# Optimization experiments

Measured on AMD Instinct MI355X. Metric: run time of the kernel, lower is better.

Reference implementation:

```python
import jax, jax.numpy as jnp
import numpy as np

GRID_SIZE = 10
SPLINE_ORDER = 3
GRID_RANGE = (0.0, 1.0)
COUNT_HARMONIC = 8


def make_grid():
    # knot vector: (grid_size + 2*spline_order + 1,) = (17,), same for every input feature
    h = (GRID_RANGE[1] - GRID_RANGE[0]) / GRID_SIZE
    return (jnp.arange(-SPLINE_ORDER, GRID_SIZE + SPLINE_ORDER + 1, dtype=jnp.float32) * h
            + GRID_RANGE[0])


def b_splines(x, grid):
    # x: (B, in) -> bases: (B, in, grid_size + spline_order) via Cox-de Boor recursion
    xg = x[..., None]                                   # (B, in, 1)
    bases = ((xg >= grid[:-1]) & (xg < grid[1:])).astype(x.dtype)  # (B, in, 16)
    for k in range(1, SPLINE_ORDER + 1):
        left = (xg - grid[:-(k + 1)]) / (grid[k:-1] - grid[:-(k + 1)]) * bases[..., :-1]
        right = (grid[k + 1:] - xg) / (grid[k + 1:] - grid[1:-k]) * bases[..., 1:]
        bases = left + right
    return bases                                        # (B, in, 13)


def kan_linear(x, base_w, spline_w, spline_scaler, grid):
    # base path: SiLU(x) @ W_base^T ; spline path: grouped weighted sum of B-spline bases
    base_out = jax.nn.silu(x) @ base_w.T                # (B, out)
    sp = b_splines(x, grid)                             # (B, in, C)
    sw = spline_w * spline_scaler[..., None]            # (out, in, C) standalone scaler
    spline_out = jnp.einsum('bic,oic->bo', sp, sw)
    return base_out + spline_out


def fft_calc(x):
    # x: (B, C, 64); two 32-sample windows, keep first count_harmonic+1 = 9 bins
    prev = jnp.fft.rfft(x[:, :, :32])[:, :, :COUNT_HARMONIC + 1]
    cur = jnp.fft.rfft(x[:, :, 32:])[:, :, :COUNT_HARMONIC + 1]
    # NOTE: original code uses the *current* window's phase twice (faithful to source)
    return jnp.concatenate(
        [jnp.abs(prev), jnp.angle(cur), jnp.abs(cur), jnp.angle(cur)], axis=-1)  # (B, C, 36)


def mlp_head(h, W1, b1, W2, b2, W3, b3):
    y = h @ W1.T + b1
    # nn.LeakyReLU(True) -> negative_slope = 1.0 -> identity (faithful to source)
    y = y @ W2.T + b2
    y = jnp.where(y >= 0, y, 0.05 * y)                  # LeakyReLU(0.05)
    y = y @ W3.T + b3
    return jax.nn.sigmoid(y)                            # (B, 1)


def setup_inputs() -> dict:
    key = jax.random.key(0)
    ks = jax.random.split(key, 20)
    B = 8192
    def n(i, shape):
        return jax.random.normal(ks[i], shape, dtype=jnp.float32)
    return {
        'x': n(0, (B, 64, 14)),
        'k1_base': n(1, (80, 504)), 'k1_spline': n(2, (80, 504, 13)), 'k1_scaler': n(3, (80, 504)),
        'k2_base': n(4, (160, 80)), 'k2_spline': n(5, (160, 80, 13)), 'k2_scaler': n(6, (160, 80)),
        'k3_base': n(7, (80, 160)), 'k3_spline': n(8, (80, 160, 13)), 'k3_scaler': n(9, (80, 160)),
        'k4_base': n(10, (40, 80)), 'k4_spline': n(11, (40, 80, 13)), 'k4_scaler': n(12, (40, 80)),
        'heads_W1': n(13, (3, 40, 40)), 'heads_b1': n(14, (3, 40)),
        'heads_W2': n(15, (3, 20, 40)), 'heads_b2': n(16, (3, 20)),
        'heads_W3': n(17, (3, 1, 20)), 'heads_b3': n(18, (3, 1)),
    }


def reference(x, k1_base, k1_spline, k1_scaler, k2_base, k2_spline, k2_scaler,
              k3_base, k3_spline, k3_scaler, k4_base, k4_spline, k4_scaler,
              heads_W1, heads_b1, heads_W2, heads_b2, heads_W3, heads_b3):
    B = x.shape[0]
    grid = make_grid()
    # original uses reshape (not transpose): (B, 64, 14) -> (B, 14, 64)
    h = x.reshape(B, x.shape[2], x.shape[1])
    h = fft_calc(h).reshape(B, -1)                      # (B, 504)
    h = kan_linear(h, k1_base, k1_spline, k1_scaler, grid)   # (B, 80)
    h = kan_linear(h, k2_base, k2_spline, k2_scaler, grid)   # (B, 160)
    h = kan_linear(h, k3_base, k3_spline, k3_scaler, grid)   # (B, 80)
    h = kan_linear(h, k4_base, k4_spline, k4_scaler, grid)   # (B, 40)
    heads = jax.vmap(lambda W1, b1, W2, b2, W3, b3: mlp_head(h, W1, b1, W2, b2, W3, b3))(
        heads_W1, heads_b1, heads_W2, heads_b2, heads_W3, heads_b3)  # (3, B, 1)
    return jnp.transpose(heads, (1, 0, 2)).reshape(B, 3)
```

## Files before the change

kernel.cpp:

```cpp
#include <hip/hip_runtime.h>
#include <math.h>


__device__ __forceinline__ float silu_f(float x) {
    return x / (1.f + __expf(-x));
}

__global__ __launch_bounds__(128) void fft_kernel(const float* __restrict__ x,
                                                  float* __restrict__ F0, int P) {
    __shared__ float xs[128 * 65];
    __shared__ float twc[288], tws[288];
    int tid = threadIdx.x;
    for (int t = tid; t < 288; t += 128) {
        int k = t >> 5, n = t & 31;
        int m = (k * n) & 31;
        float ang = -0.19634954084936207f * (float)m;
        float s, c;
        sincosf(ang, &s, &c);
        twc[t] = c; tws[t] = s;
    }
    int p0 = blockIdx.x * 128;
    for (int idx = tid; idx < 128 * 64; idx += 128) {
        int g = p0 * 64 + idx;
        float v = (g < P * 64) ? x[g] : 0.f;
        xs[(idx >> 6) * 65 + (idx & 63)] = v;
    }
    __syncthreads();
    int p = p0 + tid;
    if (p >= P) return;
    const float* row = &xs[tid * 65];
    float r[64];
#pragma unroll
    for (int n = 0; n < 64; ++n) r[n] = row[n];
    float outv[27];
#pragma unroll
    for (int k = 0; k < 9; ++k) {
        float rp = 0.f, ip = 0.f, rc = 0.f, ic = 0.f;
#pragma unroll
        for (int n = 0; n < 32; ++n) {
            float c = twc[k * 32 + n], s = tws[k * 32 + n];
            rp = fmaf(r[n], c, rp);
            ip = fmaf(r[n], s, ip);
            rc = fmaf(r[n + 32], c, rc);
            ic = fmaf(r[n + 32], s, ic);
        }
        float ap = sqrtf(fmaf(rp, rp, ip * ip));
        float ac = sqrtf(fmaf(rc, rc, ic * ic));
        float gc = atan2f(ic, rc);
        outv[k] = ap; outv[9 + k] = gc; outv[18 + k] = ac;
    }
    float* dst = &F0[(size_t)p * 27];
#pragma unroll
    for (int q = 0; q < 27; ++q) dst[q] = outv[q];
}

__device__ __forceinline__ float kval(const float* __restrict__ bw,
                                      const float* __restrict__ sw,
                                      const float* __restrict__ sc,
                                      int IN, int o, int s, int c) {
    if (c == 0) return bw[o * IN + s];
    return sw[((size_t)o * IN + s) * 13 + (c - 1)] * sc[o * IN + s];
}

__global__ void prep_all_kernel(float* __restrict__ Wf1, float* __restrict__ Wf2,
                                float* __restrict__ Wf3, float* __restrict__ Wf4,
                                float* __restrict__ W21, float* __restrict__ b21,
                                const float* k1b, const float* k1s, const float* k1c,
                                const float* k2b, const float* k2s, const float* k2c,
                                const float* k3b, const float* k3s, const float* k3c,
                                const float* k4b, const float* k4s, const float* k4c,
                                const float* W1, const float* b1,
                                const float* W2, const float* b2) {
    const int T1 = 378 * 14 * 80, T2 = 80 * 14 * 160, T3 = 160 * 14 * 80, T4 = 80 * 14 * 40;
    int id = blockIdx.x * 256 + threadIdx.x;
    if (id < T1) {
        int o = id % 80, rem = id / 80, c = rem % 14, i = rem / 14;
        int ch = i / 27, q = i % 27;
        int s1 = ch * 36 + q;
        float v = kval(k1b, k1s, k1c, 504, o, s1, c);
        if (q >= 9 && q < 18) v += kval(k1b, k1s, k1c, 504, o, s1 + 18, c);
        Wf1[id] = v;
        return;
    }
    id -= T1;
    if (id < T2) {
        int o = id % 160, rem = id / 160, c = rem % 14, i = rem / 14;
        Wf2[id] = kval(k2b, k2s, k2c, 80, o, i, c);
        return;
    }
    id -= T2;
    if (id < T3) {
        int o = id % 80, rem = id / 80, c = rem % 14, i = rem / 14;
        Wf3[id] = kval(k3b, k3s, k3c, 160, o, i, c);
        return;
    }
    id -= T3;
    if (id < T4) {
        int o = id % 40, rem = id / 40, c = rem % 14, i = rem / 14;
        Wf4[id] = kval(k4b, k4s, k4c, 80, o, i, c);
        return;
    }
    id -= T4;
    if (id < 3 * 20 * 40) {
        int k = id % 40, rem = id / 40, j = rem % 20, h = rem / 20;
        float a = 0.f;
        for (int m = 0; m < 40; ++m)
            a = fmaf(W2[(h * 20 + j) * 40 + m], W1[(h * 40 + m) * 40 + k], a);
        W21[id] = a;
    } else if (id < 3 * 20 * 40 + 60) {
        int t = id - 2400, j = t % 20, h = t / 20;
        float a = b2[h * 20 + j];
        for (int m = 0; m < 40; ++m)
            a = fmaf(W2[(h * 20 + j) * 40 + m], b1[h * 40 + m], a);
        b21[t] = a;
    }
}

template <int OUT_T, int BM, int KC>
__global__ __launch_bounds__(256, 4) void kan4_kernel(const float* __restrict__ X, int IN,
                                                      int OUTF,
                                                      const float* __restrict__ Wf,
                                                      float* __restrict__ Yp, int B) {
    constexpr int NR = 10;
    constexpr int COLS_T = OUT_T / NR;
    constexpr int ROWS_T = 256 / COLS_T;
    constexpr int MR = BM / ROWS_T;
    constexpr int NRP = 12;
    static_assert(COLS_T * NR == OUT_T, "cols");
    static_assert(ROWS_T * MR == BM, "rows");
    static_assert(KC % 2 == 0, "even KC");

    __shared__ float Ws[2 * 14 * COLS_T * NRP];
    __shared__ float Ft[2 * 14 * BM];

    const int tid = threadIdx.x;
    const int ct = tid % COLS_T, rt = tid / COLS_T;
    const int b0 = blockIdx.x * BM;
    const int ibase = blockIdx.y * KC;
    const int co = blockIdx.z * OUT_T;
    const int kk = tid / BM;
    const int rr = tid % BM;
    const bool fact = (kk < 2);

    float acc[MR][NR];
#pragma unroll
    for (int m = 0; m < MR; ++m)
#pragma unroll
        for (int n = 0; n < NR; ++n) acc[m][n] = 0.f;

    float xreg = 0.f;
    if (fact) xreg = X[(size_t)(b0 + rr) * IN + ibase + kk];

    for (int i0 = 0; i0 < KC; i0 += 2) {
        if (fact) {
            float xs = xreg;
            float* dst = &Ft[kk * 14 * BM + rr];
            dst[0] = silu_f(xs);
#pragma unroll
            for (int c = 1; c < 14; ++c) dst[c * BM] = 0.f;
            float t10 = (xs + 0.3f) * 10.f;
            if (t10 >= 0.f && t10 < 16.f) {
                int j = (int)t10;
                float u = t10 - (float)j;
                float u2 = u * u, u3 = u2 * u, v = 1.f - u;
                float B0 = v * v * v * (1.f / 6.f);
                float B1 = (3.f * u3 - 6.f * u2 + 4.f) * (1.f / 6.f);
                float B2 = (-3.f * u3 + 3.f * u2 + 3.f * u + 1.f) * (1.f / 6.f);
                float B3 = u3 * (1.f / 6.f);
                int bs = j - 3;
#pragma unroll
                for (int t = 0; t < 4; ++t) {
                    int rw = bs + t;
                    float bb = (t == 0) ? B0 : (t == 1) ? B1 : (t == 2) ? B2 : B3;
                    if (rw >= 0 && rw <= 12) dst[(1 + rw) * BM] = bb;
                }
            }
        }
        {
            const float* wsrc = Wf + (size_t)(ibase + i0) * 14 * OUTF + co;
            for (int t = tid; t < 2 * 14 * OUT_T; t += 256) {
                int o = t % OUT_T;
                int kc = t / OUT_T;
                Ws[(kc * COLS_T + o / NR) * NRP + (o % NR)] = wsrc[(size_t)kc * OUTF + o];
            }
        }
        float xn = 0.f;
        if (fact && (i0 + 2) < KC)
            xn = X[(size_t)(b0 + rr) * IN + ibase + i0 + 2 + kk];
        __syncthreads();
#pragma unroll
        for (int kc = 0; kc < 28; ++kc) {
            const float* wb = &Ws[(kc * COLS_T + ct) * NRP];
            float4 w0 = *(const float4*)(wb);
            float4 w1 = *(const float4*)(wb + 4);
            float2 w2 = *(const float2*)(wb + 8);
            float wn[NR] = {w0.x, w0.y, w0.z, w0.w, w1.x, w1.y, w1.z, w1.w, w2.x, w2.y};
            const float* fb = &Ft[kc * BM + rt * MR];
            float xm[MR];
            if constexpr (MR == 4) {
                float4 f = *(const float4*)fb;
                xm[0] = f.x; xm[1] = f.y; xm[2] = f.z; xm[3] = f.w;
            } else if constexpr (MR == 2) {
                float2 f = *(const float2*)fb;
                xm[0] = f.x; xm[1] = f.y;
            } else {
                xm[0] = fb[0];
            }
#pragma unroll
            for (int m = 0; m < MR; ++m)
#pragma unroll
                for (int n = 0; n < NR; ++n) acc[m][n] = fmaf(xm[m], wn[n], acc[m][n]);
        }
        __syncthreads();
        xreg = xn;
    }

    float* ydst = Yp + (size_t)blockIdx.y * B * OUTF;
#pragma unroll
    for (int m = 0; m < MR; ++m) {
        float* yr = ydst + (size_t)(b0 + rt * MR + m) * OUTF + co + ct * NR;
#pragma unroll
        for (int nn = 0; nn < NR / 2; ++nn)
            *(float2*)(yr + 2 * nn) = make_float2(acc[m][2 * nn], acc[m][2 * nn + 1]);
    }
}

__global__ void reduce_kernel(float* __restrict__ Y, const float* __restrict__ Yp,
                              int N, int KS) {
    int t = blockIdx.x * 256 + threadIdx.x;
    if (t >= N) return;
    float a = 0.f;
    for (int s = 0; s < KS; ++s) a += Yp[(size_t)s * N + t];
    Y[t] = a;
}

__global__ __launch_bounds__(256) void heads_kernel(const float* __restrict__ h4,
                                                    const float* __restrict__ W21,
                                                    const float* __restrict__ b21,
                                                    const float* __restrict__ W3,
                                                    const float* __restrict__ b3,
                                                    float* __restrict__ out, int B) {
    __shared__ float w21s[2400], b21s[60], w3s[60], b3s[3];
    int tid = threadIdx.x;
    for (int t = tid; t < 2400; t += 256) w21s[t] = W21[t];
    if (tid < 60) { b21s[tid] = b21[tid]; w3s[tid] = W3[tid]; }
    if (tid < 3) b3s[tid] = b3[tid];
    __syncthreads();
    int id = blockIdx.x * 256 + tid;
    if (id >= B * 3) return;
    int b = id / 3, h = id % 3;
    const float* hr = &h4[(size_t)b * 40];
    float hv[40];
#pragma unroll
    for (int m = 0; m < 40; ++m) hv[m] = hr[m];
    float z = b3s[h];
#pragma unroll
    for (int j = 0; j < 20; ++j) {
        float y = b21s[h * 20 + j];
        const float* wr = &w21s[(h * 20 + j) * 40];
#pragma unroll
        for (int m = 0; m < 40; ++m) y = fmaf(wr[m], hv[m], y);
        y = (y >= 0.f) ? y : 0.05f * y;
        z = fmaf(w3s[h * 20 + j], y, z);
    }
    out[id] = 1.f / (1.f + __expf(-z));
}

extern "C" void kernel_launch(void* const* d_in, const int* in_sizes, int n_in,
                              void* d_out, int out_size, void* d_ws, size_t ws_size,
                              hipStream_t stream) {
    const float* x   = (const float*)d_in[0];
    const float* k1b = (const float*)d_in[1];
    const float* k1s = (const float*)d_in[2];
    const float* k1c = (const float*)d_in[3];
    const float* k2b = (const float*)d_in[4];
    const float* k2s = (const float*)d_in[5];
    const float* k2c = (const float*)d_in[6];
    const float* k3b = (const float*)d_in[7];
    const float* k3s = (const float*)d_in[8];
    const float* k3c = (const float*)d_in[9];
    const float* k4b = (const float*)d_in[10];
    const float* k4s = (const float*)d_in[11];
    const float* k4c = (const float*)d_in[12];
    const float* hW1 = (const float*)d_in[13];
    const float* hb1 = (const float*)d_in[14];
    const float* hW2 = (const float*)d_in[15];
    const float* hb2 = (const float*)d_in[16];
    const float* hW3 = (const float*)d_in[17];
    const float* hb3 = (const float*)d_in[18];
    float* out = (float*)d_out;

    int B = in_sizes[0] / (64 * 14);
    int P = B * 14;

    float* ws = (float*)d_ws;
    size_t off = 0;
    float* Wf1 = ws + off; off += 378 * 14 * 80;
    float* Wf2 = ws + off; off += 80 * 14 * 160;
    float* Wf3 = ws + off; off += 160 * 14 * 80;
    float* Wf4 = ws + off; off += 80 * 14 * 40;
    float* W21 = ws + off; off += 2400;
    float* b21 = ws + off; off += 60;
    float* F0  = ws + off; off += (size_t)B * 378;
    float* h1  = ws + off; off += (size_t)B * 80;
    float* h2  = ws + off; off += (size_t)B * 160;
    float* h3  = ws + off; off += (size_t)B * 80;
    float* h4  = ws + off; off += (size_t)B * 40;
    float* Yp  = ws + off;
    size_t cap = (ws_size / 4 > off) ? (ws_size / 4 - off) : 0;

    int S1 = (cap >= (size_t)21 * B * 80)  ? 21 : 9;
    int S2 = (cap >= (size_t)8  * B * 160) ? 8  : 4;
    int S3 = (cap >= (size_t)16 * B * 80)  ? 16 : 8;
    const int S4 = 8;

    {
        int total = 378 * 14 * 80 + 80 * 14 * 160 + 160 * 14 * 80 + 80 * 14 * 40 + 2460;
        prep_all_kernel<<<(total + 255) / 256, 256, 0, stream>>>(
            Wf1, Wf2, Wf3, Wf4, W21, b21,
            k1b, k1s, k1c, k2b, k2s, k2c, k3b, k3s, k3c, k4b, k4s, k4c,
            hW1, hb1, hW2, hb2);
    }

    fft_kernel<<<(P + 127) / 128, 128, 0, stream>>>(x, F0, P);

    if (S1 == 21) kan4_kernel<80, 128, 18><<<dim3(B / 128, 21, 1), 256, 0, stream>>>(F0, 378, 80, Wf1, Yp, B);
    else          kan4_kernel<80, 128, 42><<<dim3(B / 128, 9, 1), 256, 0, stream>>>(F0, 378, 80, Wf1, Yp, B);
    reduce_kernel<<<((B * 80) + 255) / 256, 256, 0, stream>>>(h1, Yp, B * 80, S1);

    if (S2 == 8) kan4_kernel<80, 128, 10><<<dim3(B / 128, 8, 2), 256, 0, stream>>>(h1, 80, 160, Wf2, Yp, B);
    else         kan4_kernel<80, 128, 20><<<dim3(B / 128, 4, 2), 256, 0, stream>>>(h1, 80, 160, Wf2, Yp, B);
    reduce_kernel<<<((B * 160) + 255) / 256, 256, 0, stream>>>(h2, Yp, B * 160, S2);

    if (S3 == 16) kan4_kernel<80, 128, 10><<<dim3(B / 128, 16, 1), 256, 0, stream>>>(h2, 160, 80, Wf3, Yp, B);
    else          kan4_kernel<80, 128, 20><<<dim3(B / 128, 8, 1), 256, 0, stream>>>(h2, 160, 80, Wf3, Yp, B);
    reduce_kernel<<<((B * 80) + 255) / 256, 256, 0, stream>>>(h3, Yp, B * 80, S3);

    kan4_kernel<40, 64, 10><<<dim3(B / 64, S4, 1), 256, 0, stream>>>(h3, 80, 40, Wf4, Yp, B);
    reduce_kernel<<<((B * 40) + 255) / 256, 256, 0, stream>>>(h4, Yp, B * 40, S4);

    heads_kernel<<<(B * 3 + 255) / 256, 256, 0, stream>>>(h4, W21, b21, hW3, hb3, out, B);

    (void)n_in; (void)out_size;
}
```

Measured before the change: 420.7 us.

## Switch KAN layers to feature-major activations with pre-packed, register-prefetched weights

Activations are now stored feature-major (transposed), with a new transpose kernel after the FFT. The KAN kernel reads inputs coalesced along the batch and writes partial outputs transposed with vector stores. Weights are pre-packed in prep into the exact padded shared-memory tile layout, so each chunk is a straight contiguous copy that is prefetched into registers one chunk ahead. The goal is to remove strided activation loads and the index-heavy weight scatter, at the cost of an extra transpose pass, more register pressure, a dropped occupancy hint and changed split counts.

Result: faster. 389.2 us (-7.5%).

```diff
diff --git a/kernel.cpp b/kernel.cpp
--- a/kernel.cpp
+++ b/kernel.cpp
@@ -54,6 +54,20 @@
     for (int q = 0; q < 27; ++q) dst[q] = outv[q];
 }
 
+__global__ __launch_bounds__(256) void transpose_f0_kernel(const float* __restrict__ F0,
+                                                           float* __restrict__ F0T, int B) {
+    __shared__ float t[448 * 27];
+    int b0 = blockIdx.x * 32;
+    const float* src = F0 + (size_t)b0 * 14 * 27;
+    for (int idx = threadIdx.x; idx < 448 * 27; idx += 256) t[idx] = src[idx];
+    __syncthreads();
+    for (int idx = threadIdx.x; idx < 378 * 32; idx += 256) {
+        int i = idx >> 5, bb = idx & 31;
+        int ch = i / 27, q = i - ch * 27;
+        F0T[(size_t)i * B + b0 + bb] = t[(bb * 14 + ch) * 27 + q];
+    }
+}
+
 __device__ __forceinline__ float kval(const float* __restrict__ bw,
                                       const float* __restrict__ sw,
                                       const float* __restrict__ sc,
@@ -62,8 +76,8 @@
     return sw[((size_t)o * IN + s) * 13 + (c - 1)] * sc[o * IN + s];
 }
 
-__global__ void prep_all_kernel(float* __restrict__ Wf1, float* __restrict__ Wf2,
-                                float* __restrict__ Wf3, float* __restrict__ Wf4,
+__global__ void prep_all_kernel(float* __restrict__ Wfp1, float* __restrict__ Wfp2,
+                                float* __restrict__ Wfp3, float* __restrict__ Wfp4,
                                 float* __restrict__ W21, float* __restrict__ b21,
                                 const float* k1b, const float* k1s, const float* k1c,
                                 const float* k2b, const float* k2s, const float* k2c,
@@ -71,34 +85,40 @@
                                 const float* k4b, const float* k4s, const float* k4c,
                                 const float* W1, const float* b1,
                                 const float* W2, const float* b2) {
-    const int T1 = 378 * 14 * 80, T2 = 80 * 14 * 160, T3 = 160 * 14 * 80, T4 = 80 * 14 * 40;
+    const int T1 = 189 * 2688, T2 = 40 * 2 * 2688, T3 = 80 * 2688, T4 = 40 * 1344;
     int id = blockIdx.x * 256 + threadIdx.x;
     if (id < T1) {
-        int o = id % 80, rem = id / 80, c = rem % 14, i = rem / 14;
-        int ch = i / 27, q = i % 27;
-        int s1 = ch * 36 + q;
-        float v = kval(k1b, k1s, k1c, 504, o, s1, c);
-        if (q >= 9 && q < 18) v += kval(k1b, k1s, k1c, 504, o, s1 + 18, c);
-        Wf1[id] = v;
-        return;
+        int jg = id / 2688, t = id % 2688;
+        int kc = t / 96, t2 = t % 96, ct = t2 / 12, r = t2 % 12;
+        int i = 2 * jg + kc / 14, c = kc % 14, o = ct * 10 + r;
+        float v = 0.f;
+        if (r < 10) {
+            int ch = i / 27, q = i - ch * 27, s1 = ch * 36 + q;
+            v = kval(k1b, k1s, k1c, 504, o, s1, c);
+            if (q >= 9 && q < 18) v += kval(k1b, k1s, k1c, 504, o, s1 + 18, c);
+        }
+        Wfp1[id] = v; return;
     }
     id -= T1;
     if (id < T2) {
-        int o = id % 160, rem = id / 160, c = rem % 14, i = rem / 14;
-        Wf2[id] = kval(k2b, k2s, k2c, 80, o, i, c);
-        return;
+        int jg = id / (2 * 2688), rem = id % (2 * 2688), half = rem / 2688, t = rem % 2688;
+        int kc = t / 96, t2 = t % 96, ct = t2 / 12, r = t2 % 12;
+        int i = 2 * jg + kc / 14, c = kc % 14, o = half * 80 + ct * 10 + r;
+        Wfp2[id] = (r < 10) ? kval(k2b, k2s, k2c, 80, o, i, c) : 0.f; return;
     }
     id -= T2;
     if (id < T3) {
-        int o = id % 80, rem = id / 80, c = rem % 14, i = rem / 14;
-        Wf3[id] = kval(k3b, k3s, k3c, 160, o, i, c);
-        return;
+        int jg = id / 2688, t = id % 2688;
+        int kc = t / 96, t2 = t % 96, ct = t2 / 12, r = t2 % 12;
+        int i = 2 * jg + kc / 14, c = kc % 14, o = ct * 10 + r;
+        Wfp3[id] = (r < 10) ? kval(k3b, k3s, k3c, 160, o, i, c) : 0.f; return;
     }
     id -= T3;
     if (id < T4) {
-        int o = id % 40, rem = id / 40, c = rem % 14, i = rem / 14;
-        Wf4[id] = kval(k4b, k4s, k4c, 80, o, i, c);
-        return;
+        int jg = id / 1344, t = id % 1344;
+        int kc = t / 48, t2 = t % 48, ct = t2 / 12, r = t2 % 12;
+        int i = 2 * jg + kc / 14, c = kc % 14, o = ct * 10 + r;
+        Wfp4[id] = (r < 10) ? kval(k4b, k4s, k4c, 80, o, i, c) : 0.f; return;
     }
     id -= T4;
     if (id < 3 * 20 * 40) {
@@ -116,31 +136,33 @@
     }
 }
 
-template <int OUT_T, int BM, int KC>
-__global__ __launch_bounds__(256, 4) void kan4_kernel(const float* __restrict__ X, int IN,
-                                                      int OUTF,
-                                                      const float* __restrict__ Wf,
-                                                      float* __restrict__ Yp, int B) {
+template <int OUT_T, int KC, int NHALF>
+__global__ __launch_bounds__(256) void kan5_kernel(const float* __restrict__ XT, int B,
+                                                   const float* __restrict__ Wfp,
+                                                   float* __restrict__ YpT, int OUTF) {
+    constexpr int BM = 128;
     constexpr int NR = 10;
     constexpr int COLS_T = OUT_T / NR;
     constexpr int ROWS_T = 256 / COLS_T;
     constexpr int MR = BM / ROWS_T;
-    constexpr int NRP = 12;
+    constexpr int NW = 28 * COLS_T * 12;
+    constexpr int NCH = KC / 2;
+    constexpr int WSTG = (NW + 255) / 256;
     static_assert(COLS_T * NR == OUT_T, "cols");
     static_assert(ROWS_T * MR == BM, "rows");
     static_assert(KC % 2 == 0, "even KC");
 
-    __shared__ float Ws[2 * 14 * COLS_T * NRP];
-    __shared__ float Ft[2 * 14 * BM];
+    __shared__ float Ws[NW];
+    __shared__ float Ft[28 * BM];
 
     const int tid = threadIdx.x;
-    const int ct = tid % COLS_T, rt = tid / COLS_T;
+    const int rt = tid % ROWS_T, ct = tid / ROWS_T;
     const int b0 = blockIdx.x * BM;
-    const int ibase = blockIdx.y * KC;
-    const int co = blockIdx.z * OUT_T;
-    const int kk = tid / BM;
-    const int rr = tid % BM;
-    const bool fact = (kk < 2);
+    const int s = blockIdx.y;
+    const int half = blockIdx.z;
+    const int ibase = s * KC;
+    const int kk = tid >> 7;
+    const int rr = tid & 127;
 
     float acc[MR][NR];
 #pragma unroll
@@ -148,11 +170,23 @@
 #pragma unroll
         for (int n = 0; n < NR; ++n) acc[m][n] = 0.f;
 
-    float xreg = 0.f;
-    if (fact) xreg = X[(size_t)(b0 + rr) * IN + ibase + kk];
-
-    for (int i0 = 0; i0 < KC; i0 += 2) {
-        if (fact) {
+    const size_t wbase0 = ((size_t)(ibase / 2) * NHALF + half) * NW;
+    float wreg[WSTG];
+#pragma unroll
+    for (int u = 0; u < WSTG; ++u) {
+        int t = tid + u * 256;
+        wreg[u] = (t < NW) ? Wfp[wbase0 + t] : 0.f;
+    }
+    float xreg = XT[(size_t)(ibase + kk) * B + b0 + rr];
+
+    for (int j = 0; j < NCH; ++j) {
+        __syncthreads();
+#pragma unroll
+        for (int u = 0; u < WSTG; ++u) {
+            int t = tid + u * 256;
+            if (t < NW) Ws[t] = wreg[u];
+        }
+        {
             float xs = xreg;
             float* dst = &Ft[kk * 14 * BM + rr];
             dst[0] = silu_f(xs);
@@ -160,14 +194,14 @@
             for (int c = 1; c < 14; ++c) dst[c * BM] = 0.f;
             float t10 = (xs + 0.3f) * 10.f;
             if (t10 >= 0.f && t10 < 16.f) {
-                int j = (int)t10;
-                float u = t10 - (float)j;
+                int jj = (int)t10;
+                float u = t10 - (float)jj;
                 float u2 = u * u, u3 = u2 * u, v = 1.f - u;
                 float B0 = v * v * v * (1.f / 6.f);
                 float B1 = (3.f * u3 - 6.f * u2 + 4.f) * (1.f / 6.f);
                 float B2 = (-3.f * u3 + 3.f * u2 + 3.f * u + 1.f) * (1.f / 6.f);
                 float B3 = u3 * (1.f / 6.f);
-                int bs = j - 3;
+                int bs = jj - 3;
 #pragma unroll
                 for (int t = 0; t < 4; ++t) {
                     int rw = bs + t;
@@ -176,21 +210,19 @@
                 }
             }
         }
-        {
-            const float* wsrc = Wf + (size_t)(ibase + i0) * 14 * OUTF + co;
-            for (int t = tid; t < 2 * 14 * OUT_T; t += 256) {
-                int o = t % OUT_T;
-                int kc = t / OUT_T;
-                Ws[(kc * COLS_T + o / NR) * NRP + (o % NR)] = wsrc[(size_t)kc * OUTF + o];
+        if (j + 1 < NCH) {
+            const size_t wb = wbase0 + (size_t)(j + 1) * NHALF * NW;
+#pragma unroll
+            for (int u = 0; u < WSTG; ++u) {
+                int t = tid + u * 256;
+                if (t < NW) wreg[u] = Wfp[wb + t];
             }
-        }
-        float xn = 0.f;
-        if (fact && (i0 + 2) < KC)
-            xn = X[(size_t)(b0 + rr) * IN + ibase + i0 + 2 + kk];
+            xreg = XT[(size_t)(ibase + 2 * (j + 1) + kk) * B + b0 + rr];
+        }
         __syncthreads();
 #pragma unroll
         for (int kc = 0; kc < 28; ++kc) {
-            const float* wb = &Ws[(kc * COLS_T + ct) * NRP];
+            const float* wb = &Ws[(kc * COLS_T + ct) * 12];
             float4 w0 = *(const float4*)(wb);
             float4 w1 = *(const float4*)(wb + 4);
             float2 w2 = *(const float2*)(wb + 8);
@@ -200,28 +232,25 @@
             if constexpr (MR == 4) {
                 float4 f = *(const float4*)fb;
                 xm[0] = f.x; xm[1] = f.y; xm[2] = f.z; xm[3] = f.w;
-            } else if constexpr (MR == 2) {
+            } else {
                 float2 f = *(const float2*)fb;
                 xm[0] = f.x; xm[1] = f.y;
-            } else {
-                xm[0] = fb[0];
             }
 #pragma unroll
             for (int m = 0; m < MR; ++m)
 #pragma unroll
                 for (int n = 0; n < NR; ++n) acc[m][n] = fmaf(xm[m], wn[n], acc[m][n]);
         }
-        __syncthreads();
-        xreg = xn;
-    }
-
-    float* ydst = Yp + (size_t)blockIdx.y * B * OUTF;
-#pragma unroll
-    for (int m = 0; m < MR; ++m) {
-        float* yr = ydst + (size_t)(b0 + rt * MR + m) * OUTF + co + ct * NR;
-#pragma unroll
-        for (int nn = 0; nn < NR / 2; ++nn)
-            *(float2*)(yr + 2 * nn) = make_float2(acc[m][2 * nn], acc[m][2 * nn + 1]);
+    }
+
+    float* yd = YpT + (size_t)s * OUTF * B + (size_t)(half * OUT_T) * B;
+#pragma unroll
+    for (int n = 0; n < NR; ++n) {
+        float* p = yd + (size_t)(ct * NR + n) * B + b0 + rt * MR;
+        if constexpr (MR == 4)
+            *(float4*)p = make_float4(acc[0][n], acc[1][n], acc[2][n], acc[3][n]);
+        else
+            *(float2*)p = make_float2(acc[0][n], acc[1][n]);
     }
 }
 
@@ -234,7 +263,7 @@
     Y[t] = a;
 }
 
-__global__ __launch_bounds__(256) void heads_kernel(const float* __restrict__ h4,
+__global__ __launch_bounds__(256) void heads_kernel(const float* __restrict__ h4T,
                                                     const float* __restrict__ W21,
                                                     const float* __restrict__ b21,
                                                     const float* __restrict__ W3,
@@ -249,10 +278,9 @@
     int id = blockIdx.x * 256 + tid;
     if (id >= B * 3) return;
     int b = id / 3, h = id % 3;
-    const float* hr = &h4[(size_t)b * 40];
     float hv[40];
 #pragma unroll
-    for (int m = 0; m < 40; ++m) hv[m] = hr[m];
+    for (int m = 0; m < 40; ++m) hv[m] = h4T[(size_t)m * B + b];
     float z = b3s[h];
 #pragma unroll
     for (int j = 0; j < 20; ++j) {
@@ -295,51 +323,58 @@
 
     float* ws = (float*)d_ws;
     size_t off = 0;
-    float* Wf1 = ws + off; off += 378 * 14 * 80;
-    float* Wf2 = ws + off; off += 80 * 14 * 160;
-    float* Wf3 = ws + off; off += 160 * 14 * 80;
-    float* Wf4 = ws + off; off += 80 * 14 * 40;
-    float* W21 = ws + off; off += 2400;
-    float* b21 = ws + off; off += 60;
-    float* F0  = ws + off; off += (size_t)B * 378;
-    float* h1  = ws + off; off += (size_t)B * 80;
-    float* h2  = ws + off; off += (size_t)B * 160;
-    float* h3  = ws + off; off += (size_t)B * 80;
-    float* h4  = ws + off; off += (size_t)B * 40;
-    float* Yp  = ws + off;
+    float* Wfp1 = ws + off; off += 189 * 2688;
+    float* Wfp2 = ws + off; off += 40 * 2 * 2688;
+    float* Wfp3 = ws + off; off += 80 * 2688;
+    float* Wfp4 = ws + off; off += 40 * 1344;
+    float* W21  = ws + off; off += 2400;
+    float* b21  = ws + off; off += 60;
+    float* F0T  = ws + off; off += (size_t)B * 378;
+    float* h1T  = ws + off; off += (size_t)B * 80;
+    float* h2T  = ws + off; off += (size_t)B * 160;
+    float* h3T  = ws + off; off += (size_t)B * 80;
+    float* h4T  = ws + off; off += (size_t)B * 40;
+    float* F0   = ws + off;
+    float* Yp   = ws + off;
     size_t cap = (ws_size / 4 > off) ? (ws_size / 4 - off) : 0;
-
-    int S1 = (cap >= (size_t)21 * B * 80)  ? 21 : 9;
-    int S2 = (cap >= (size_t)8  * B * 160) ? 8  : 4;
-    int S3 = (cap >= (size_t)16 * B * 80)  ? 16 : 8;
-    const int S4 = 8;
+    int S1 = (cap >= (size_t)21 * B * 80) ? 21 : (cap >= (size_t)9 * B * 80) ? 9
+           : (cap >= (size_t)7 * B * 80) ? 7 : 3;
+    int S2 = (cap >= (size_t)10 * B * 160) ? 10 : (cap >= (size_t)5 * B * 160) ? 5 : 2;
+    int S3 = (cap >= (size_t)20 * B * 80) ? 20 : (cap >= (size_t)8 * B * 80) ? 8 : 4;
+    int S4 = (cap >= (size_t)10 * B * 40) ? 10 : 2;
 
     {
-        int total = 378 * 14 * 80 + 80 * 14 * 160 + 160 * 14 * 80 + 80 * 14 * 40 + 2460;
+        int total = 189 * 2688 + 40 * 2 * 2688 + 80 * 2688 + 40 * 1344 + 2460;
         prep_all_kernel<<<(total + 255) / 256, 256, 0, stream>>>(
-            Wf1, Wf2, Wf3, Wf4, W21, b21,
+            Wfp1, Wfp2, Wfp3, Wfp4, W21, b21,
             k1b, k1s, k1c, k2b, k2s, k2c, k3b, k3s, k3c, k4b, k4s, k4c,
             hW1, hb1, hW2, hb2);
     }
 
     fft_kernel<<<(P + 127) / 128, 128, 0, stream>>>(x, F0, P);
-
-    if (S1 == 21) kan4_kernel<80, 128, 18><<<dim3(B / 128, 21, 1), 256, 0, stream>>>(F0, 378, 80, Wf1, Yp, B);
-    else          kan4_kernel<80, 128, 42><<<dim3(B / 128, 9, 1), 256, 0, stream>>>(F0, 378, 80, Wf1, Yp, B);
-    reduce_kernel<<<((B * 80) + 255) / 256, 256, 0, stream>>>(h1, Yp, B * 80, S1);
-
-    if (S2 == 8) kan4_kernel<80, 128, 10><<<dim3(B / 128, 8, 2), 256, 0, stream>>>(h1, 80, 160, Wf2, Yp, B);
-    else         kan4_kernel<80, 128, 20><<<dim3(B / 128, 4, 2), 256, 0, stream>>>(h1, 80, 160, Wf2, Yp, B);
-    reduce_kernel<<<((B * 160) + 255) / 256, 256, 0, stream>>>(h2, Yp, B * 160, S2);
-
-    if (S3 == 16) kan4_kernel<80, 128, 10><<<dim3(B / 128, 16, 1), 256, 0, stream>>>(h2, 160, 80, Wf3, Yp, B);
-    else          kan4_kernel<80, 128, 20><<<dim3(B / 128, 8, 1), 256, 0, stream>>>(h2, 160, 80, Wf3, Yp, B);
-    reduce_kernel<<<((B * 80) + 255) / 256, 256, 0, stream>>>(h3, Yp, B * 80, S3);
-
-    kan4_kernel<40, 64, 10><<<dim3(B / 64, S4, 1), 256, 0, stream>>>(h3, 80, 40, Wf4, Yp, B);
-    reduce_kernel<<<((B * 40) + 255) / 256, 256, 0, stream>>>(h4, Yp, B * 40, S4);
-
-    heads_kernel<<<(B * 3 + 255) / 256, 256, 0, stream>>>(h4, W21, b21, hW3, hb3, out, B);
+    transpose_f0_kernel<<<B / 32, 256, 0, stream>>>(F0, F0T, B);
+
+    if (S1 == 21)     kan5_kernel<80, 18, 1><<<dim3(B / 128, 21, 1), 256, 0, stream>>>(F0T, B, Wfp1, Yp, 80);
+    else if (S1 == 9) kan5_kernel<80, 42, 1><<<dim3(B / 128, 9, 1), 256, 0, stream>>>(F0T, B, Wfp1, Yp, 80);
+    else if (S1 == 7) kan5_kernel<80, 54, 1><<<dim3(B / 128, 7, 1), 256, 0, stream>>>(F0T, B, Wfp1, Yp, 80);
+    else              kan5_kernel<80, 126, 1><<<dim3(B / 128, 3, 1), 256, 0, stream>>>(F0T, B, Wfp1, Yp, 80);
+    reduce_kernel<<<((B * 80) + 255) / 256, 256, 0, stream>>>(h1T, Yp, B * 80, S1);
+
+    if (S2 == 10)     kan5_kernel<80, 8, 2><<<dim3(B / 128, 10, 2), 256, 0, stream>>>(h1T, B, Wfp2, Yp, 160);
+    else if (S2 == 5) kan5_kernel<80, 16, 2><<<dim3(B / 128, 5, 2), 256, 0, stream>>>(h1T, B, Wfp2, Yp, 160);
+    else              kan5_kernel<80, 40, 2><<<dim3(B / 128, 2, 2), 256, 0, stream>>>(h1T, B, Wfp2, Yp, 160);
+    reduce_kernel<<<((B * 160) + 255) / 256, 256, 0, stream>>>(h2T, Yp, B * 160, S2);
+
+    if (S3 == 20)     kan5_kernel<80, 8, 1><<<dim3(B / 128, 20, 1), 256, 0, stream>>>(h2T, B, Wfp3, Yp, 80);
+    else if (S3 == 8) kan5_kernel<80, 20, 1><<<dim3(B / 128, 8, 1), 256, 0, stream>>>(h2T, B, Wfp3, Yp, 80);
+    else              kan5_kernel<80, 40, 1><<<dim3(B / 128, 4, 1), 256, 0, stream>>>(h2T, B, Wfp3, Yp, 80);
+    reduce_kernel<<<((B * 80) + 255) / 256, 256, 0, stream>>>(h3T, Yp, B * 80, S3);
+
+    if (S4 == 10) kan5_kernel<40, 8, 1><<<dim3(B / 128, 10, 1), 256, 0, stream>>>(h3T, B, Wfp4, Yp, 40);
+    else          kan5_kernel<40, 40, 1><<<dim3(B / 128, 2, 1), 256, 0, stream>>>(h3T, B, Wfp4, Yp, 40);
+    reduce_kernel<<<((B * 40) + 255) / 256, 256, 0, stream>>>(h4T, Yp, B * 40, S4);
+
+    heads_kernel<<<(B * 3 + 255) / 256, 256, 0, stream>>>(h4T, W21, b21, hW3, hb3, out, B);
 
     (void)n_in; (void)out_size;
 }
```
